# Optimization experiments

Measured on AMD Instinct MI355X. Metric: run time of the kernel, lower is better.

The kernel has to match this reference:

```python
import jax, jax.numpy as jnp
import numpy as np


def _forward(x, wc, we, Wb1, bb1, Wb2, bb2, Wr1, br1, Wr2, br2,
             Wq1, bq1, Wq2, bq2, Wq3, bq3, Wo1, bo1, Wo2, bo2, Wo3, bo3, scale):
    bs, c, h, w = x.shape
    Hs, Ws = scale * h, scale * w
    fh = (jnp.arange(Hs, dtype=jnp.float32) + 0.5) / scale
    fw = (jnp.arange(Ws, dtype=jnp.float32) + 0.5) / scale
    coor_h = fh - jnp.floor(fh + 0.001) - 0.5  # [Hs] fractional phase
    coor_w = fw - jnp.floor(fw + 0.001) - 0.5  # [Ws]
    ones_hw = jnp.ones((Hs, Ws), jnp.float32)
    meta = jnp.stack([ones_hw, ones_hw / scale,
                      jnp.broadcast_to(coor_h[:, None], (Hs, Ws)),
                      jnp.broadcast_to(coor_w[None, :], (Hs, Ws))], 0)  # [4,Hs,Ws]
    chan_mean = x.mean(axis=(0, 2, 3))  # [c]
    chan_scale = jnp.concatenate([chan_mean[:, None], jnp.ones((c, 3), jnp.float32)], axis=1)  # [c,4]
    inp = meta[None] * chan_scale[:, :, None, None]  # [c,4,Hs,Ws]

    # body: 1x1x1 Conv3d over spectral-channel axis c
    lin = lambda W, b, t: jnp.einsum('oc,cfhw->ofhw', W, t) + b[:, None, None, None]
    emb = jax.nn.relu(lin(Wb2, bb2, jax.nn.relu(lin(Wb1, bb1, inp))))  # [c,4,Hs,Ws]

    # offset head: Conv2d 1x1 with batch = c, features = 4 -> 2
    lin2 = lambda W, b, t: jnp.einsum('of,cfhw->cohw', W, t) + b[None, :, None, None]
    off = lin2(Wo3, bo3, jax.nn.relu(lin2(Wo2, bo2, jax.nn.relu(lin2(Wo1, bo1, emb)))))  # [c,2,Hs,Ws]

    # routing_1: Conv3d over c -> 1 channel, sigmoid
    r = jax.nn.sigmoid(lin(Wr2, br2, jax.nn.relu(lin(Wr1, br1, emb))))[0]  # [4,Hs,Ws]
    # routing_2: Conv2d 1x1 over the 4 meta-features -> E experts
    lin3 = lambda W, b, t: jnp.einsum('of,fhw->ohw', W, t) + b[:, None, None]
    rw = jax.nn.sigmoid(lin3(Wq3, bq3, jax.nn.relu(lin3(Wq2, bq2, jax.nn.relu(lin3(Wq1, bq1, r))))))  # [E,Hs,Ws]

    # per-channel offset grid_sample (bilinear, zeros padding, align_corners=True)
    px0 = fw - 0.5  # [Ws] base source x coord
    py0 = fh - 0.5  # [Hs]

    def sample(img, offx, offy):  # img [bs,h,w]; off* [Hs,Ws]
        px = px0[None, :] + offx
        py = py0[:, None] + offy
        x0 = jnp.floor(px); y0 = jnp.floor(py)
        wx = px - x0; wy = py - y0
        x0i = x0.astype(jnp.int32); y0i = y0.astype(jnp.int32)
        def g(yi, xi):
            v = ((xi >= 0) & (xi <= w - 1) & (yi >= 0) & (yi <= h - 1)).astype(img.dtype)
            return img[:, jnp.clip(yi, 0, h - 1), jnp.clip(xi, 0, w - 1)] * v[None]
        return (g(y0i, x0i) * ((1 - wy) * (1 - wx))[None]
                + g(y0i, x0i + 1) * ((1 - wy) * wx)[None]
                + g(y0i + 1, x0i) * (wy * (1 - wx))[None]
                + g(y0i + 1, x0i + 1) * (wy * wx)[None])

    fea0 = jax.vmap(lambda xi, oi: sample(xi, oi[0], oi[1]),
                    in_axes=(1, 0), out_axes=1)(x, off)  # [bs,c,Hs,Ws]

    # per-pixel expert-mixed compress/expand: (sum_e r_e Wc_e) f then (sum_e r_e We_e)
    mid = jnp.einsum('ehw,ekc,bchw->bkhw', rw, wc, fea0)   # [bs,c//8,Hs,Ws]
    out = jnp.einsum('ehw,eck,bkhw->bchw', rw, we, mid)    # [bs,c,Hs,Ws]
    return out + fea0


def setup_inputs() -> dict:
    key = jax.random.key(0)
    ks = jax.random.split(key, 32)
    bs, c, h, w = 4, 64, 64, 64
    E, k = 4, c // 8
    s = 0.05
    d = {
        'x': jax.random.normal(ks[0], (bs, c, h, w), jnp.float32),
        'wc': jax.random.normal(ks[1], (E, k, c), jnp.float32) * s,
        'we': jax.random.normal(ks[2], (E, c, k), jnp.float32) * s,
        'Wb1': jax.random.normal(ks[3], (c, c), jnp.float32) * s,
        'bb1': jax.random.normal(ks[4], (c,), jnp.float32) * s,
        'Wb2': jax.random.normal(ks[5], (c, c), jnp.float32) * s,
        'bb2': jax.random.normal(ks[6], (c,), jnp.float32) * s,
        'Wr1': jax.random.normal(ks[7], (64, c), jnp.float32) * s,
        'br1': jax.random.normal(ks[8], (64,), jnp.float32) * s,
        'Wr2': jax.random.normal(ks[9], (1, 64), jnp.float32) * s,
        'br2': jax.random.normal(ks[10], (1,), jnp.float32) * s,
        'Wq1': jax.random.normal(ks[11], (64, 4), jnp.float32) * s,
        'bq1': jax.random.normal(ks[12], (64,), jnp.float32) * s,
        'Wq2': jax.random.normal(ks[13], (64, 64), jnp.float32) * s,
        'bq2': jax.random.normal(ks[14], (64,), jnp.float32) * s,
        'Wq3': jax.random.normal(ks[15], (E, 64), jnp.float32) * s,
        'bq3': jax.random.normal(ks[16], (E,), jnp.float32) * s,
        'Wo1': jax.random.normal(ks[17], (64, 4), jnp.float32) * s,
        'bo1': jax.random.normal(ks[18], (64,), jnp.float32) * s,
        'Wo2': jax.random.normal(ks[19], (64, 64), jnp.float32) * s,
        'bo2': jax.random.normal(ks[20], (64,), jnp.float32) * s,
        'Wo3': jax.random.normal(ks[21], (2, 64), jnp.float32) * s,
        'bo3': jax.random.normal(ks[22], (2,), jnp.float32) * s,
        'scale': 4,
    }
    return d


def reference(x, wc, we, Wb1, bb1, Wb2, bb2, Wr1, br1, Wr2, br2,
              Wq1, bq1, Wq2, bq2, Wq3, bq3, Wo1, bo1, Wo2, bo2, Wo3, bo3, scale):
    return _forward(x, wc, we, Wb1, bb1, Wb2, bb2, Wr1, br1, Wr2, br2,
                    Wq1, bq1, Wq2, bq2, Wq3, bq3, Wo1, bo1, Wo2, bo2, Wo3, bo3, int(scale))
```

## Files before the change

kernel.cpp:

```cpp
#include <hip/hip_runtime.h>


__device__ __forceinline__ float relu_(float v){ return fmaxf(v, 0.f); }
__device__ __forceinline__ float sigm_(float v){ return 1.f/(1.f + __expf(-v)); }

__global__ void k_mean(const float* __restrict__ x, float* __restrict__ ws) {
  const int ch = blockIdx.x, b = blockIdx.y, t = threadIdx.x;
  const float4* p = reinterpret_cast<const float4*>(x + (size_t)(b*64 + ch)*4096);
  float4 v0 = p[t], v1 = p[t+256], v2 = p[t+512], v3 = p[t+768];
  float s = ((v0.x+v0.y)+(v0.z+v0.w)) + ((v1.x+v1.y)+(v1.z+v1.w))
          + ((v2.x+v2.y)+(v2.z+v2.w)) + ((v3.x+v3.y)+(v3.z+v3.w));
  __shared__ float red[256];
  red[t] = s; __syncthreads();
  for (int off = 128; off > 0; off >>= 1) {
    if (t < off) red[t] += red[t + off];
    __syncthreads();
  }
  if (t == 0) ws[b*64 + ch] = red[0];
}

__launch_bounds__(256)
__global__ void k_phase(const float* __restrict__ wc, const float* __restrict__ we,
    const float* __restrict__ Wb1, const float* __restrict__ bb1,
    const float* __restrict__ Wb2, const float* __restrict__ bb2,
    const float* __restrict__ Wr1, const float* __restrict__ br1,
    const float* __restrict__ Wr2, const float* __restrict__ br2,
    const float* __restrict__ Wq1, const float* __restrict__ bq1,
    const float* __restrict__ Wq2, const float* __restrict__ bq2,
    const float* __restrict__ Wq3, const float* __restrict__ bq3,
    const float* __restrict__ Wo1, const float* __restrict__ bo1,
    const float* __restrict__ Wo2, const float* __restrict__ bo2,
    const float* __restrict__ Wo3, const float* __restrict__ bo3,
    float* __restrict__ ws)
{
  const int p = blockIdx.x, pi = p >> 2, pj = p & 3;
  const int t = threadIdx.x;
  const float chv = 0.25f*pi - 0.375f, cwv = 0.25f*pj - 0.375f;

  __shared__ float WbL1[64*66];
  __shared__ float WbL2[64*66];
  __shared__ float WrL1[64*66];
  __shared__ float WqL2[64*66];
  __shared__ __align__(16) float Wo2L[4096];
  __shared__ __align__(16) float Wo1L[256];
  __shared__ __align__(16) float wcL[2048];
  __shared__ __align__(16) float weL[2048];
  __shared__ float Wo3L[128];
  __shared__ float Wq1L[256], Wq3L[256];
  __shared__ float Wr2L[64];
  __shared__ float bb1L[64], bb2L[64], br1L[64], bq1L[64], bq2L[64];
  __shared__ float bo1L[64], bo2L[64];

  __shared__ float meanL[64];
  __shared__ __align__(16) float t1L[64][4];
  __shared__ __align__(16) float embL[64][4];
  __shared__ __align__(16) float rpL[64][4];
  __shared__ float r4[4];
  __shared__ float q1L[64], q2L[64];
  __shared__ float rwL[4];
  __shared__ float oxL[64][4], oyL[64][4];
  __shared__ float oxF[64], oyF[64];

  {
    const float* srcs[4] = {Wb1, Wb2, Wr1, Wq2};
    float* dsts[4] = {WbL1, WbL2, WrL1, WqL2};
    for (int m = 0; m < 4; ++m) {
      const float4* W4 = reinterpret_cast<const float4*>(srcs[m]);
      float* WL = dsts[m];
      for (int v = t; v < 1024; v += 256) {
        float4 d = W4[v];
        const int r = v >> 4, c = (v & 15) << 2;
        float* q = &WL[r*66 + c];
        q[0] = d.x; q[1] = d.y; q[2] = d.z; q[3] = d.w;
      }
    }
    for (int v = t; v < 1024; v += 256)
      reinterpret_cast<float4*>(Wo2L)[v] = reinterpret_cast<const float4*>(Wo2)[v];
    for (int v = t; v < 512; v += 256) {
      reinterpret_cast<float4*>(wcL)[v] = reinterpret_cast<const float4*>(wc)[v];
      reinterpret_cast<float4*>(weL)[v] = reinterpret_cast<const float4*>(we)[v];
    }
    if (t < 64) {
      reinterpret_cast<float4*>(Wo1L)[t] = reinterpret_cast<const float4*>(Wo1)[t];
      reinterpret_cast<float4*>(Wq1L)[t] = reinterpret_cast<const float4*>(Wq1)[t];
      reinterpret_cast<float4*>(Wq3L)[t] = reinterpret_cast<const float4*>(Wq3)[t];
      bb1L[t] = bb1[t]; bb2L[t] = bb2[t]; br1L[t] = br1[t];
      bq1L[t] = bq1[t]; bq2L[t] = bq2[t];
      bo1L[t] = bo1[t]; bo2L[t] = bo2[t];
      Wr2L[t] = Wr2[t];
      const float* wsp = ws;
      meanL[t] = (wsp[t] + wsp[64+t] + wsp[128+t] + wsp[192+t]) * (1.f/16384.f);
    }
    if (t >= 64 && t < 192) Wo3L[t-64] = Wo3[t-64];
  }
  __syncthreads();

  if (t < 64) {
    float a0 = 0.f, as = 0.f;
    const float* row = &WbL1[t*66];
    #pragma unroll 8
    for (int c = 0; c < 64; ++c) { float w = row[c]; a0 += w*meanL[c]; as += w; }
    float bb = bb1L[t];
    t1L[t][0] = relu_(a0 + bb);
    t1L[t][1] = relu_(0.25f*as + bb);
    t1L[t][2] = relu_(chv*as + bb);
    t1L[t][3] = relu_(cwv*as + bb);
  }
  __syncthreads();
  if (t < 64) {
    float bb = bb2L[t];
    float e0=bb,e1=bb,e2=bb,e3=bb;
    const float* row = &WbL2[t*66];
    #pragma unroll 8
    for (int c = 0; c < 64; ++c) {
      float w = row[c];
      float4 tv = *reinterpret_cast<const float4*>(&t1L[c][0]);
      e0 += w*tv.x; e1 += w*tv.y; e2 += w*tv.z; e3 += w*tv.w;
    }
    embL[t][0]=relu_(e0); embL[t][1]=relu_(e1); embL[t][2]=relu_(e2); embL[t][3]=relu_(e3);
  }
  __syncthreads();
  if (t < 64) {
    float bb = br1L[t];
    float p0=bb,p1=bb,p2=bb,p3=bb;
    const float* row = &WrL1[t*66];
    #pragma unroll 8
    for (int c = 0; c < 64; ++c) {
      float w = row[c];
      float4 ev = *reinterpret_cast<const float4*>(&embL[c][0]);
      p0 += w*ev.x; p1 += w*ev.y; p2 += w*ev.z; p3 += w*ev.w;
    }
    rpL[t][0]=relu_(p0); rpL[t][1]=relu_(p1); rpL[t][2]=relu_(p2); rpL[t][3]=relu_(p3);
  }
  __syncthreads();
  if (t < 4) {
    float acc = br2[0];
    #pragma unroll 8
    for (int c = 0; c < 64; ++c) acc += Wr2L[c]*rpL[c][t];
    r4[t] = sigm_(acc);
  }
  __syncthreads();
  if (t < 64) {
    float acc = bq1L[t];
    #pragma unroll
    for (int f = 0; f < 4; ++f) acc += Wq1L[t*4+f]*r4[f];
    q1L[t] = relu_(acc);
  }
  __syncthreads();
  if (t < 64) {
    float acc = bq2L[t];
    const float* row = &WqL2[t*66];
    #pragma unroll 8
    for (int c = 0; c < 64; ++c) acc += row[c]*q1L[c];
    q2L[t] = relu_(acc);
  }
  __syncthreads();
  if (t < 4) {
    float acc = bq3[t];
    #pragma unroll 8
    for (int c = 0; c < 64; ++c) acc += Wq3L[t*64+c]*q2L[c];
    rwL[t] = sigm_(acc);
  }
  __syncthreads();

  {
    const int ch = t & 63, q = t >> 6;
    const float4 e = *reinterpret_cast<const float4*>(&embL[ch][0]);
    float v1[64];
    #pragma unroll
    for (int o = 0; o < 64; ++o) {
      float4 w = *reinterpret_cast<const float4*>(&Wo1L[o*4]);
      v1[o] = relu_(w.x*e.x + w.y*e.y + w.z*e.z + w.w*e.w + bo1L[o]);
    }
    float ox = 0.f, oy = 0.f;
    for (int o = q*16; o < q*16+16; ++o) {
      float acc = bo2L[o];
      const float4* row = reinterpret_cast<const float4*>(&Wo2L[o*64]);
      #pragma unroll
      for (int k = 0; k < 16; ++k) {
        float4 w = row[k];
        acc += w.x*v1[4*k+0] + w.y*v1[4*k+1] + w.z*v1[4*k+2] + w.w*v1[4*k+3];
      }
      acc = relu_(acc);
      ox += Wo3L[o]*acc;
      oy += Wo3L[64+o]*acc;
    }
    oxL[ch][q] = ox; oyL[ch][q] = oy;
  }
  __syncthreads();
  if (t < 64) {
    oxF[t] = oxL[t][0]+oxL[t][1]+oxL[t][2]+oxL[t][3] + bo3[0];
    oyF[t] = oyL[t][0]+oyL[t][1]+oyL[t][2]+oyL[t][3] + bo3[1];
  }
  __syncthreads();

  if (t < 64) {
    const float B = 0.25f*pj - 0.375f + oxF[t];
    const float bx = floorf(B);
    const float wx = B - bx;
    float4 pr;
    pr.x = __int_as_float((int)bx);
    pr.y = 1.f - wx;
    pr.z = wx;
    pr.w = 0.f;
    *reinterpret_cast<float4*>(ws + 256 + (p*64 + t)*4) = pr;
  }

  {
    const float r0 = rwL[0], r1 = rwL[1], r2 = rwL[2], r3 = rwL[3];
    for (int idx = t; idx < 1024; idx += 256) {
      const int ch = idx >> 4, k = idx & 15;
      float v;
      if (k < 8) {
        v = r0*wcL[(0*8+k)*64+ch] + r1*wcL[(1*8+k)*64+ch]
          + r2*wcL[(2*8+k)*64+ch] + r3*wcL[(3*8+k)*64+ch];
      } else {
        const int kk = k - 8;
        v = r0*weL[(0*64+ch)*8+kk] + r1*weL[(1*64+ch)*8+kk]
          + r2*weL[(2*64+ch)*8+kk] + r3*weL[(3*64+ch)*8+kk];
      }
      ws[4352 + (p*64+ch)*16 + k] = v;
    }
  }

  {
    const int ch = t & 63, iq = t >> 6;
    const float oy = oyF[ch];
    float* dst = ws + 20736 + (p*64 + ch)*1024 + iq*256;
    for (int n = 0; n < 64; ++n) {
      const int i = iq*64 + n;
      const float py = i*0.25f - 0.375f + oy;
      const float fy = floorf(py);
      const float wy = py - fy;
      const int y0 = (int)fy, y1 = y0 + 1;
      const int y0c = min(max(y0, 0), 63), y1c = min(max(y1, 0), 63);
      const float wy0 = ((unsigned)y0 <= 63u) ? (1.f - wy) : 0.f;
      const float wy1 = ((unsigned)y1 <= 63u) ? wy : 0.f;
      float4 yi;
      yi.x = __int_as_float(ch*4096 + y0c*64);
      yi.y = __int_as_float(ch*4096 + y1c*64);
      yi.z = wy0; yi.w = wy1;
      reinterpret_cast<float4*>(dst)[n] = yi;
    }
  }
}

__launch_bounds__(256, 4)
__global__ void k_main(const float* __restrict__ x, const float* __restrict__ ws,
                       float* __restrict__ out) {
  const int i = blockIdx.x;
  const int b = blockIdx.y;
  const int w = __builtin_amdgcn_readfirstlane((int)(threadIdx.x >> 6));
  const int l = threadIdx.x & 63;
  const int p = (i & 3)*4 + w;

  const float* __restrict__ prm = ws + 256   + p*256;
  const float* __restrict__ wmx = ws + 4352  + p*1024;
  const float* __restrict__ yif = ws + 20736 + p*65536 + i*4;
  const float* __restrict__ xb  = x + (size_t)b*262144;

  float fea[64];
  float m0=0.f,m1=0.f,m2=0.f,m3=0.f,m4=0.f,m5=0.f,m6=0.f,m7=0.f;

  #pragma unroll
  for (int ch = 0; ch < 64; ++ch) {
    const float4 pr = *reinterpret_cast<const float4*>(prm + ch*4);
    const float4 yi = *reinterpret_cast<const float4*>(yif + ch*1024);
    const float4 wa = *reinterpret_cast<const float4*>(wmx + ch*16);
    const float4 wb = *reinterpret_cast<const float4*>(wmx + ch*16 + 4);
    const int x0 = l + __float_as_int(pr.x);
    const int x1 = x0 + 1;
    const int x0c = min(max(x0, 0), 63);
    const int x1c = min(max(x1, 0), 63);
    const float u0 = ((unsigned)x0 <= 63u) ? pr.y : 0.f;
    const float u1 = ((unsigned)x1 <= 63u) ? pr.z : 0.f;
    const int rb0 = __float_as_int(yi.x), rb1 = __float_as_int(yi.y);
    const float g00 = xb[rb0 + x0c], g01 = xb[rb0 + x1c];
    const float g10 = xb[rb1 + x0c], g11 = xb[rb1 + x1c];
    const float f0 = g00*u0 + g01*u1;
    const float f1 = g10*u0 + g11*u1;
    const float fv = f0*yi.z + f1*yi.w;
    fea[ch] = fv;
    m0 += wa.x*fv; m1 += wa.y*fv; m2 += wa.z*fv; m3 += wa.w*fv;
    m4 += wb.x*fv; m5 += wb.y*fv; m6 += wb.z*fv; m7 += wb.w*fv;
  }

  float* __restrict__ ob = out + (size_t)b*4194304;
  const int joff = i*256 + 4*l + w;
  #pragma unroll
  for (int ch = 0; ch < 64; ++ch) {
    const float4 wa = *reinterpret_cast<const float4*>(wmx + ch*16 + 8);
    const float4 wb = *reinterpret_cast<const float4*>(wmx + ch*16 + 12);
    float acc = fea[ch];
    acc += wa.x*m0 + wa.y*m1 + wa.z*m2 + wa.w*m3;
    acc += wb.x*m4 + wb.y*m5 + wb.z*m6 + wb.w*m7;
    ob[joff + ch*65536] = acc;
  }
}

extern "C" void kernel_launch(void* const* d_in, const int* in_sizes, int n_in,
                              void* d_out, int out_size, void* d_ws, size_t ws_size,
                              hipStream_t stream) {
  const float* x   = (const float*)d_in[0];
  const float* wc  = (const float*)d_in[1];
  const float* we  = (const float*)d_in[2];
  const float* Wb1 = (const float*)d_in[3];
  const float* bb1 = (const float*)d_in[4];
  const float* Wb2 = (const float*)d_in[5];
  const float* bb2 = (const float*)d_in[6];
  const float* Wr1 = (const float*)d_in[7];
  const float* br1 = (const float*)d_in[8];
  const float* Wr2 = (const float*)d_in[9];
  const float* br2 = (const float*)d_in[10];
  const float* Wq1 = (const float*)d_in[11];
  const float* bq1 = (const float*)d_in[12];
  const float* Wq2 = (const float*)d_in[13];
  const float* bq2 = (const float*)d_in[14];
  const float* Wq3 = (const float*)d_in[15];
  const float* bq3 = (const float*)d_in[16];
  const float* Wo1 = (const float*)d_in[17];
  const float* bo1 = (const float*)d_in[18];
  const float* Wo2 = (const float*)d_in[19];
  const float* bo2 = (const float*)d_in[20];
  const float* Wo3 = (const float*)d_in[21];
  const float* bo3 = (const float*)d_in[22];
  float* ws  = (float*)d_ws;
  float* out = (float*)d_out;

  k_mean<<<dim3(64, 4), 256, 0, stream>>>(x, ws);
  k_phase<<<16, 256, 0, stream>>>(wc, we, Wb1, bb1, Wb2, bb2, Wr1, br1, Wr2, br2,
                                  Wq1, bq1, Wq2, bq2, Wq3, bq3,
                                  Wo1, bo1, Wo2, bo2, Wo3, bo3, ws);
  k_main<<<dim3(256, 4), 256, 0, stream>>>(x, ws, out);
}
```

Baseline: 197.7 us.

## Pad input into zero-bordered workspace and stage output writes through LDS transpose

k_mean now also copies each input channel into a zero-padded 66x72 buffer in the workspace. Because the borders are zero, k_main no longer needs x-bound clamps or validity masks. The per-row y-index table is re-laid out so that all channels for a row are contiguous, and the x-offset is baked into the row base pointers. k_main's output now goes through a swizzled shared-memory tile so that each wave writes contiguous 64-float spans instead of stride-4 scattered stores, at the cost of extra barriers and a larger workspace.

After: 181.1 us. -8.4%, faster.

```diff
diff --git a/kernel.cpp b/kernel.cpp
--- a/kernel.cpp
+++ b/kernel.cpp
@@ -6,8 +6,9 @@
 
 __global__ void k_mean(const float* __restrict__ x, float* __restrict__ ws) {
   const int ch = blockIdx.x, b = blockIdx.y, t = threadIdx.x;
-  const float4* p = reinterpret_cast<const float4*>(x + (size_t)(b*64 + ch)*4096);
-  float4 v0 = p[t], v1 = p[t+256], v2 = p[t+512], v3 = p[t+768];
+  const float* xp = x + (size_t)(b*64 + ch)*4096;
+  const float4* p4 = reinterpret_cast<const float4*>(xp);
+  float4 v0 = p4[t], v1 = p4[t+256], v2 = p4[t+512], v3 = p4[t+768];
   float s = ((v0.x+v0.y)+(v0.z+v0.w)) + ((v1.x+v1.y)+(v1.z+v1.w))
           + ((v2.x+v2.y)+(v2.z+v2.w)) + ((v3.x+v3.y)+(v3.z+v3.w));
   __shared__ float red[256];
@@ -17,6 +18,22 @@
     __syncthreads();
   }
   if (t == 0) ws[b*64 + ch] = red[0];
+
+  float* dst = ws + 1069312 + (size_t)(b*64 + ch)*4752;
+  if (t < 66) {
+    float4* drow = reinterpret_cast<float4*>(dst + t*72);
+    const float4 z = make_float4(0.f, 0.f, 0.f, 0.f);
+    if (t == 0 || t == 65) {
+      #pragma unroll
+      for (int q = 0; q < 18; ++q) drow[q] = z;
+    } else {
+      const float4* srow = reinterpret_cast<const float4*>(xp + (t-1)*64);
+      drow[0] = z;
+      #pragma unroll
+      for (int q = 0; q < 16; ++q) drow[1+q] = srow[q];
+      drow[17] = z;
+    }
+  }
 }
 
 __launch_bounds__(256)
@@ -60,6 +77,7 @@
   __shared__ float rwL[4];
   __shared__ float oxL[64][4], oyL[64][4];
   __shared__ float oxF[64], oyF[64];
+  __shared__ int bxS[64];
 
   {
     const float* srcs[4] = {Wb1, Wb2, Wr1, Wq2};
@@ -196,15 +214,15 @@
 
   if (t < 64) {
     const float B = 0.25f*pj - 0.375f + oxF[t];
-    const float bx = floorf(B);
-    const float wx = B - bx;
-    float4 pr;
-    pr.x = __int_as_float((int)bx);
-    pr.y = 1.f - wx;
-    pr.z = wx;
-    pr.w = 0.f;
-    *reinterpret_cast<float4*>(ws + 256 + (p*64 + t)*4) = pr;
-  }
+    const float bxf = floorf(B);
+    const float wx = B - bxf;
+    int bx = (int)bxf;
+    bx = min(max(bx, -4), 3);
+    ws[256 + (p*64 + t)*2 + 0] = 1.f - wx;
+    ws[256 + (p*64 + t)*2 + 1] = wx;
+    bxS[t] = bx;
+  }
+  __syncthreads();
 
   {
     const float r0 = rwL[0], r1 = rwL[1], r2 = rwL[2], r3 = rwL[3];
@@ -226,75 +244,83 @@
   {
     const int ch = t & 63, iq = t >> 6;
     const float oy = oyF[ch];
-    float* dst = ws + 20736 + (p*64 + ch)*1024 + iq*256;
+    const int chbase = ch*4752 + 4 + bxS[ch];
+    float4* dst = reinterpret_cast<float4*>(ws + 20736 + (size_t)p*65536);
     for (int n = 0; n < 64; ++n) {
       const int i = iq*64 + n;
       const float py = i*0.25f - 0.375f + oy;
       const float fy = floorf(py);
       const float wy = py - fy;
       const int y0 = (int)fy, y1 = y0 + 1;
-      const int y0c = min(max(y0, 0), 63), y1c = min(max(y1, 0), 63);
+      const int y0c = min(max(y0, -1), 64), y1c = min(max(y1, -1), 64);
       const float wy0 = ((unsigned)y0 <= 63u) ? (1.f - wy) : 0.f;
       const float wy1 = ((unsigned)y1 <= 63u) ? wy : 0.f;
       float4 yi;
-      yi.x = __int_as_float(ch*4096 + y0c*64);
-      yi.y = __int_as_float(ch*4096 + y1c*64);
+      yi.x = __int_as_float(chbase + (y0c+1)*72);
+      yi.y = __int_as_float(chbase + (y1c+1)*72);
       yi.z = wy0; yi.w = wy1;
-      reinterpret_cast<float4*>(dst)[n] = yi;
+      dst[i*64 + ch] = yi;
     }
   }
 }
 
 __launch_bounds__(256, 4)
-__global__ void k_main(const float* __restrict__ x, const float* __restrict__ ws,
-                       float* __restrict__ out) {
+__global__ void k_main(const float* __restrict__ ws, float* __restrict__ out) {
   const int i = blockIdx.x;
   const int b = blockIdx.y;
   const int w = __builtin_amdgcn_readfirstlane((int)(threadIdx.x >> 6));
   const int l = threadIdx.x & 63;
   const int p = (i & 3)*4 + w;
 
-  const float* __restrict__ prm = ws + 256   + p*256;
+  const float* __restrict__ xw  = ws + 256   + p*128;
   const float* __restrict__ wmx = ws + 4352  + p*1024;
-  const float* __restrict__ yif = ws + 20736 + p*65536 + i*4;
-  const float* __restrict__ xb  = x + (size_t)b*262144;
+  const float* __restrict__ yrc = ws + 20736 + (size_t)p*65536 + (size_t)i*256;
+  const float* __restrict__ xpb = ws + 1069312 + (size_t)b*304128;
+
+  __shared__ float tile[4096];
 
   float fea[64];
   float m0=0.f,m1=0.f,m2=0.f,m3=0.f,m4=0.f,m5=0.f,m6=0.f,m7=0.f;
 
   #pragma unroll
   for (int ch = 0; ch < 64; ++ch) {
-    const float4 pr = *reinterpret_cast<const float4*>(prm + ch*4);
-    const float4 yi = *reinterpret_cast<const float4*>(yif + ch*1024);
+    const float4 yi = *reinterpret_cast<const float4*>(yrc + ch*4);
+    const float wx0 = xw[ch*2], wx1 = xw[ch*2+1];
     const float4 wa = *reinterpret_cast<const float4*>(wmx + ch*16);
     const float4 wb = *reinterpret_cast<const float4*>(wmx + ch*16 + 4);
-    const int x0 = l + __float_as_int(pr.x);
-    const int x1 = x0 + 1;
-    const int x0c = min(max(x0, 0), 63);
-    const int x1c = min(max(x1, 0), 63);
-    const float u0 = ((unsigned)x0 <= 63u) ? pr.y : 0.f;
-    const float u1 = ((unsigned)x1 <= 63u) ? pr.z : 0.f;
     const int rb0 = __float_as_int(yi.x), rb1 = __float_as_int(yi.y);
-    const float g00 = xb[rb0 + x0c], g01 = xb[rb0 + x1c];
-    const float g10 = xb[rb1 + x0c], g11 = xb[rb1 + x1c];
-    const float f0 = g00*u0 + g01*u1;
-    const float f1 = g10*u0 + g11*u1;
+    const float g00 = xpb[rb0 + l], g01 = xpb[rb0 + l + 1];
+    const float g10 = xpb[rb1 + l], g11 = xpb[rb1 + l + 1];
+    const float f0 = g00*wx0 + g01*wx1;
+    const float f1 = g10*wx0 + g11*wx1;
     const float fv = f0*yi.z + f1*yi.w;
     fea[ch] = fv;
     m0 += wa.x*fv; m1 += wa.y*fv; m2 += wa.z*fv; m3 += wa.w*fv;
     m4 += wb.x*fv; m5 += wb.y*fv; m6 += wb.z*fv; m7 += wb.w*fv;
   }
 
-  float* __restrict__ ob = out + (size_t)b*4194304;
-  const int joff = i*256 + 4*l + w;
+  float* __restrict__ ob = out + (size_t)b*4194304 + i*256;
+  const int sw = (w & 1) << 4;
   #pragma unroll
-  for (int ch = 0; ch < 64; ++ch) {
-    const float4 wa = *reinterpret_cast<const float4*>(wmx + ch*16 + 8);
-    const float4 wb = *reinterpret_cast<const float4*>(wmx + ch*16 + 12);
-    float acc = fea[ch];
-    acc += wa.x*m0 + wa.y*m1 + wa.z*m2 + wa.w*m3;
-    acc += wb.x*m4 + wb.y*m5 + wb.z*m6 + wb.w*m7;
-    ob[joff + ch*65536] = acc;
+  for (int c4 = 0; c4 < 4; ++c4) {
+    #pragma unroll
+    for (int cc = 0; cc < 16; ++cc) {
+      const int ch = c4*16 + cc;
+      const float4 wa = *reinterpret_cast<const float4*>(wmx + ch*16 + 8);
+      const float4 wb = *reinterpret_cast<const float4*>(wmx + ch*16 + 12);
+      float acc = fea[ch];
+      acc += wa.x*m0 + wa.y*m1 + wa.z*m2 + wa.w*m3;
+      acc += wb.x*m4 + wb.y*m5 + wb.z*m6 + wb.w*m7;
+      tile[cc*256 + w*64 + (l ^ sw)] = acc;
+    }
+    __syncthreads();
+    #pragma unroll
+    for (int cc = 0; cc < 16; ++cc) {
+      const int ch = c4*16 + cc;
+      const float v = tile[cc*256 + (l&3)*64 + ((w*16 + (l>>2)) ^ ((l&1)<<4))];
+      ob[ch*65536 + w*64 + l] = v;
+    }
+    __syncthreads();
   }
 }
 
@@ -331,5 +357,5 @@
   k_phase<<<16, 256, 0, stream>>>(wc, we, Wb1, bb1, Wb2, bb2, Wr1, br1, Wr2, br2,
                                   Wq1, bq1, Wq2, bq2, Wq3, bq3,
                                   Wo1, bo1, Wo2, bo2, Wo3, bo3, ws);
-  k_main<<<dim3(256, 4), 256, 0, stream>>>(x, ws, out);
+  k_main<<<dim3(256, 4), 256, 0, stream>>>(ws, out);
 }
```
